# Kernel tuning notes

Measured on AMD Instinct MI355X. Metric: run time of the kernel, lower is better.

The kernel has to match this reference:

```python
import jax, jax.numpy as jnp
import numpy as np

N = 50000   # nodes
E = 800000  # edges (avg degree 16)
D = 2048    # resnet50 feature dim
C = 256     # layer_size
NEG_SLOPE = 0.2


def setup_inputs() -> dict:
    key = jax.random.key(0)
    ks = jax.random.split(key, 16)
    s = 0.02
    inp = {
        'x': jax.random.normal(ks[0], (N, D), jnp.float32),
        'edge_index': jax.random.randint(ks[1], (2, E), 0, N, dtype=jnp.int32),
        # GATConv layer 1 (in=D, out=C, heads=1)
        'W1': jax.random.normal(ks[2], (D, C), jnp.float32) * s,
        'a_src1': jax.random.normal(ks[3], (C,), jnp.float32) * s,
        'a_dst1': jax.random.normal(ks[4], (C,), jnp.float32) * s,
        'b1': jnp.zeros((C,), jnp.float32),
        # GATConv layer 2 (in=C, out=C)
        'W2': jax.random.normal(ks[5], (C, C), jnp.float32) * s,
        'a_src2': jax.random.normal(ks[6], (C,), jnp.float32) * s,
        'a_dst2': jax.random.normal(ks[7], (C,), jnp.float32) * s,
        'b2': jnp.zeros((C,), jnp.float32),
        # EdgePredictor: lin1 (2C -> C), lin2 (C -> 1)
        'Wp1': jax.random.normal(ks[8], (2 * C, C), jnp.float32) * s,
        'bp1': jnp.zeros((C,), jnp.float32),
        'wp2': jax.random.normal(ks[9], (C,), jnp.float32) * s,
        'bp2': jnp.zeros((), jnp.float32),
    }
    return inp


def gat_layer(x, src, dst, W, a_src, a_dst, b, n_nodes):
    # PyG GATConv, heads=1, concat=True: message flows src -> dst,
    # softmax over incoming edges of each dst node.
    h = x @ W                                   # [N, C]
    e = jax.nn.leaky_relu((h @ a_src)[src] + (h @ a_dst)[dst], NEG_SLOPE)  # [E]
    emax = jax.ops.segment_max(e, dst, num_segments=n_nodes)
    ex = jnp.exp(e - emax[dst])
    denom = jax.ops.segment_sum(ex, dst, num_segments=n_nodes)
    alpha = ex / (denom[dst] + 1e-16)           # [E]
    out = jax.ops.segment_sum(h[src] * alpha[:, None], dst, num_segments=n_nodes)
    return out + b


def reference(x, edge_index, W1, a_src1, a_dst1, b1, W2, a_src2, a_dst2, b2,
              Wp1, bp1, wp2, bp2):
    src, dst = edge_index[0], edge_index[1]
    # GATConv default add_self_loops=True
    loops = jnp.arange(N, dtype=src.dtype)
    src_sl = jnp.concatenate([src, loops])
    dst_sl = jnp.concatenate([dst, loops])

    h = gat_layer(x, src_sl, dst_sl, W1, a_src1, a_dst1, b1, N)
    h = gat_layer(h, src_sl, dst_sl, W2, a_src2, a_dst2, b2, N)

    # edge predictor on the ORIGINAL edge_index (no self loops)
    xe = jnp.concatenate([h[src], h[dst]], axis=-1)       # [E, 2C]
    z = jax.nn.relu(xe @ Wp1 + bp1)                        # [E, C]  (dropout: eval mode)
    return z @ wp2 + bp2                                   # [E]
```

## Files before the change

### kernel.cpp

```cpp
#include <hip/hip_runtime.h>
#include <hip/hip_bf16.h>
#include <stdint.h>

#define NNODES 50000
#define NEDGES 800000
#define DIN    2048
#define CDIM   256
#define ELOOP  (NEDGES + NNODES)

using bf16x8 = __attribute__((ext_vector_type(8))) short;
using f32x4  = __attribute__((ext_vector_type(4))) float;
using gvoid  = __attribute__((address_space(1))) const void;
using lvoid  = __attribute__((address_space(3))) void;

__device__ __forceinline__ float bf2f(uint16_t u) {
    union { uint32_t i; float f; } v; v.i = (uint32_t)u << 16; return v.f;
}
__device__ __forceinline__ uint16_t f2bf(float f) {
    union { float f; uint32_t i; } v; v.f = f;
    uint32_t i = v.i;
    return (uint16_t)((i + 0x7FFFu + ((i >> 16) & 1u)) >> 16);
}

#define BM 128
#define BN 128
#define BK 32

#define WAITVM(N) asm volatile("s_waitcnt vmcnt(" #N ")" ::: "memory")

#define ROWDOT_EPILOGUE()                                                     \
    if (s_src) {                                                              \
        float av[4], dv[4];                                                   \
        for (int nt2 = 0; nt2 < 4; ++nt2) {                                   \
            int gn = bn + wn + nt2 * 16 + lm;                                 \
            av[nt2] = asrc[gn];                                               \
            dv[nt2] = adst[gn];                                               \
        }                                                                     \
        for (int mt = 0; mt < 4; ++mt)                                        \
            for (int r = 0; r < 4; ++r) {                                     \
                float ps = 0.f, pd = 0.f;                                     \
                for (int nt2 = 0; nt2 < 4; ++nt2) {                           \
                    float v = acc[mt][nt2][r];                                \
                    ps += v * av[nt2];                                        \
                    pd += v * dv[nt2];                                        \
                }                                                             \
                for (int d = 1; d < 16; d <<= 1) {                            \
                    ps += __shfl_xor(ps, d);                                  \
                    pd += __shfl_xor(pd, d);                                  \
                }                                                             \
                if (lm == 0) {                                                \
                    int gm = bm + wm + mt * 16 + lq * 4 + r;                  \
                    if (gm < M) {                                             \
                        atomicAdd(&s_src[gm], ps);                            \
                        atomicAdd(&s_dst[gm], pd);                            \
                    }                                                         \
                }                                                             \
            }                                                                 \
    }

__global__ __launch_bounds__(256)
void gemm_bt(const uint16_t* __restrict__ A, const uint16_t* __restrict__ Bt,
             uint16_t* __restrict__ C, const float* __restrict__ bias,
             const float* __restrict__ asrc, const float* __restrict__ adst,
             float* __restrict__ s_src, float* __restrict__ s_dst,
             int M, int N, int K)
{
    __shared__ __align__(16) uint16_t lA[3][BM * BK];
    __shared__ __align__(16) uint16_t lB[3][BN * BK];
    const int tid  = threadIdx.x;
    const int wave = tid >> 6;
    const int lane = tid & 63;
    const int lm = lane & 15, lq = lane >> 4;
    const int bm = blockIdx.x * BM;
    const int bn = blockIdx.y * BN;
    const int wm = (wave >> 1) * 64;
    const int wn = (wave & 1) * 64;

    f32x4 acc[4][4];
    for (int i = 0; i < 4; ++i)
        for (int j = 0; j < 4; ++j)
            acc[i][j] = (f32x4)0.0f;

    auto stage = [&](int buf, int k0) {
        for (int j = 0; j < 2; ++j) {
            int c = j * 256 + wave * 64 + lane;
            int row = c >> 2, cc = c & 3;
            int gr = bm + row; if (gr >= M) gr = M - 1;
            const uint16_t* gp = A + (size_t)gr * K + k0 + cc * 8;
            __builtin_amdgcn_global_load_lds((gvoid*)gp,
                (lvoid*)(lA[buf] + (size_t)(j * 256 + wave * 64) * 8), 16, 0, 0);
        }
        for (int j = 0; j < 2; ++j) {
            int c = j * 256 + wave * 64 + lane;
            int row = c >> 2, cc = c & 3;
            const uint16_t* gp = Bt + (size_t)(bn + row) * K + k0 + cc * 8;
            __builtin_amdgcn_global_load_lds((gvoid*)gp,
                (lvoid*)(lB[buf] + (size_t)(j * 256 + wave * 64) * 8), 16, 0, 0);
        }
    };

    const int ntiles = K / BK;
    stage(0, 0);
    stage(1, BK);
    WAITVM(4);
    __builtin_amdgcn_s_barrier();

    for (int t = 0; t < ntiles; ++t) {
        const int cur = t % 3;
        if (t + 2 < ntiles) stage((t + 2) % 3, (t + 2) * BK);

        bf16x8 af[4], bfr[4];
        for (int mt = 0; mt < 4; ++mt)
            af[mt] = *(const bf16x8*)(lA[cur] + (wm + mt * 16 + lm) * BK + lq * 8);
        for (int nt2 = 0; nt2 < 4; ++nt2)
            bfr[nt2] = *(const bf16x8*)(lB[cur] + (wn + nt2 * 16 + lm) * BK + lq * 8);

        for (int mt = 0; mt < 4; ++mt)
            for (int nt2 = 0; nt2 < 4; ++nt2)
                acc[mt][nt2] = __builtin_amdgcn_mfma_f32_16x16x32_bf16(
                    af[mt], bfr[nt2], acc[mt][nt2], 0, 0, 0);

        if (t + 1 < ntiles) {
            if (t + 2 < ntiles) WAITVM(4);
            else                WAITVM(0);
            __builtin_amdgcn_s_barrier();
        }
    }

    for (int mt = 0; mt < 4; ++mt) {
        for (int nt2 = 0; nt2 < 4; ++nt2) {
            int gn = bn + wn + nt2 * 16 + lm;
            float badd = bias ? bias[gn] : 0.0f;
            for (int r = 0; r < 4; ++r) {
                int gm = bm + wm + mt * 16 + lq * 4 + r;
                if (gm < M)
                    C[(size_t)gm * N + gn] = f2bf(acc[mt][nt2][r] + badd);
            }
        }
    }

    ROWDOT_EPILOGUE();
}

__global__ __launch_bounds__(256)
void gemm_f32_bt(const float* __restrict__ A, const uint16_t* __restrict__ Bt,
                 uint16_t* __restrict__ C,
                 const float* __restrict__ asrc, const float* __restrict__ adst,
                 float* __restrict__ s_src, float* __restrict__ s_dst,
                 int M, int N, int K)
{
    __shared__ __align__(16) float    lA[3][BM * BK];
    __shared__ __align__(16) uint16_t lB[3][BN * BK];
    const int tid  = threadIdx.x;
    const int wave = tid >> 6;
    const int lane = tid & 63;
    const int lm = lane & 15, lq = lane >> 4;
    const int bm = blockIdx.x * BM;
    const int bn = blockIdx.y * BN;
    const int wm = (wave >> 1) * 64;
    const int wn = (wave & 1) * 64;

    f32x4 acc[4][4];
    for (int i = 0; i < 4; ++i)
        for (int j = 0; j < 4; ++j)
            acc[i][j] = (f32x4)0.0f;

    auto stage = [&](int buf, int k0) {
        for (int j = 0; j < 4; ++j) {
            int c = j * 256 + wave * 64 + lane;
            int row = c >> 3;
            int lc  = (c & 7) ^ (row & 7);
            int gr = bm + row; if (gr >= M) gr = M - 1;
            const float* gp = A + (size_t)gr * K + k0 + lc * 4;
            __builtin_amdgcn_global_load_lds((gvoid*)gp,
                (lvoid*)(lA[buf] + (size_t)(j * 256 + wave * 64) * 4), 16, 0, 0);
        }
        for (int j = 0; j < 2; ++j) {
            int c = j * 256 + wave * 64 + lane;
            int row = c >> 2, cc = c & 3;
            const uint16_t* gp = Bt + (size_t)(bn + row) * K + k0 + cc * 8;
            __builtin_amdgcn_global_load_lds((gvoid*)gp,
                (lvoid*)(lB[buf] + (size_t)(j * 256 + wave * 64) * 8), 16, 0, 0);
        }
    };

    const int ntiles = K / BK;
    stage(0, 0);
    stage(1, BK);
    WAITVM(6);
    __builtin_amdgcn_s_barrier();

    for (int t = 0; t < ntiles; ++t) {
        const int cur = t % 3;
        if (t + 2 < ntiles) stage((t + 2) % 3, (t + 2) * BK);

        bf16x8 af[4], bfr[4];
        for (int mt = 0; mt < 4; ++mt) {
            int r = wm + mt * 16 + lm;
            int s0 = (lq * 2)     ^ (r & 7);
            int s1 = (lq * 2 + 1) ^ (r & 7);
            f32x4 a0 = *(const f32x4*)(lA[cur] + r * BK + s0 * 4);
            f32x4 a1 = *(const f32x4*)(lA[cur] + r * BK + s1 * 4);
            union { uint32_t u[4]; bf16x8 v; } t2;
            float x0 = a0[0], x1 = a0[1], x2 = a0[2], x3 = a0[3];
            float y0 = a1[0], y1 = a1[1], y2 = a1[2], y3 = a1[3];
            asm("v_cvt_pk_bf16_f32 %0, %1, %2" : "=v"(t2.u[0]) : "v"(x0), "v"(x1));
            asm("v_cvt_pk_bf16_f32 %0, %1, %2" : "=v"(t2.u[1]) : "v"(x2), "v"(x3));
            asm("v_cvt_pk_bf16_f32 %0, %1, %2" : "=v"(t2.u[2]) : "v"(y0), "v"(y1));
            asm("v_cvt_pk_bf16_f32 %0, %1, %2" : "=v"(t2.u[3]) : "v"(y2), "v"(y3));
            af[mt] = t2.v;
        }
        for (int nt2 = 0; nt2 < 4; ++nt2)
            bfr[nt2] = *(const bf16x8*)(lB[cur] + (wn + nt2 * 16 + lm) * BK + lq * 8);

        for (int mt = 0; mt < 4; ++mt)
            for (int nt2 = 0; nt2 < 4; ++nt2)
                acc[mt][nt2] = __builtin_amdgcn_mfma_f32_16x16x32_bf16(
                    af[mt], bfr[nt2], acc[mt][nt2], 0, 0, 0);

        if (t + 1 < ntiles) {
            if (t + 2 < ntiles) WAITVM(6);
            else                WAITVM(0);
            __builtin_amdgcn_s_barrier();
        }
    }

    for (int mt = 0; mt < 4; ++mt) {
        for (int nt2 = 0; nt2 < 4; ++nt2) {
            int gn = bn + wn + nt2 * 16 + lm;
            for (int r = 0; r < 4; ++r) {
                int gm = bm + wm + mt * 16 + lq * 4 + r;
                if (gm < M)
                    C[(size_t)gm * N + gn] = f2bf(acc[mt][nt2][r]);
            }
        }
    }

    ROWDOT_EPILOGUE();
}

__global__ __launch_bounds__(256)
void transpose_cvt_kernel(const float* __restrict__ W,
                          uint16_t* __restrict__ Wt, int K, int N)
{
    __shared__ float tile[32][33];
    const int k0 = blockIdx.x * 32, n0 = blockIdx.y * 32;
    const int tx = threadIdx.x & 31, ty = threadIdx.x >> 5;
    for (int r = 0; r < 32; r += 8)
        tile[ty + r][tx] = W[(size_t)(k0 + ty + r) * N + n0 + tx];
    __syncthreads();
    for (int r = 0; r < 32; r += 8)
        Wt[(size_t)(n0 + ty + r) * K + k0 + tx] = f2bf(tile[tx][ty + r]);
}

__global__ void bias512_kernel(const float* __restrict__ bp1,
                               float* __restrict__ bias512)
{
    int i = blockIdx.x * 256 + threadIdx.x;
    if (i < 512) bias512[i] = (i < 256) ? bp1[i] : 0.0f;
}

__global__ void count_kernel(const int* __restrict__ ei, int* __restrict__ rs)
{
    int i = blockIdx.x * 256 + threadIdx.x;
    if (i >= ELOOP) return;
    int dst = (i < NEDGES) ? ei[NEDGES + i] : (i - NEDGES);
    atomicAdd(&rs[dst + 1], 1);
}

__global__ __launch_bounds__(1024)
void scan_part_kernel(int* __restrict__ rs, int* __restrict__ bsum)
{
    __shared__ int wsum[16];
    const int b = blockIdx.x, tid = threadIdx.x, lane = tid & 63, w = tid >> 6;
    int i = b * 1024 + tid;
    int v = (i <= NNODES) ? rs[i] : 0;
    int s = v;
    for (int d = 1; d < 64; d <<= 1) {
        int t = __shfl_up(s, d);
        if (lane >= d) s += t;
    }
    if (lane == 63) wsum[w] = s;
    __syncthreads();
    if (tid < 16) {
        int x = wsum[tid];
        for (int d = 1; d < 16; d <<= 1) {
            int t = __shfl_up(x, d);
            if (tid >= d) x += t;
        }
        wsum[tid] = x;
    }
    __syncthreads();
    int incl = s + (w > 0 ? wsum[w - 1] : 0);
    if (i <= NNODES) rs[i] = incl;
    if (tid == 1023) bsum[b] = incl;
}

__global__ void scan_bsum_kernel(int* __restrict__ bsum, int nb)
{
    int tid = threadIdx.x;
    int v = (tid < nb) ? bsum[tid] : 0;
    for (int d = 1; d < 64; d <<= 1) {
        int t = __shfl_up(v, d);
        if (tid >= d) v += t;
    }
    if (tid < nb) bsum[tid] = v;
}

__global__ __launch_bounds__(1024)
void scan_add_kernel(const int* __restrict__ bsum, int* __restrict__ rs,
                     int* __restrict__ cursor)
{
    int b = blockIdx.x;
    int i = b * 1024 + threadIdx.x;
    int add = b ? bsum[b - 1] : 0;
    if (i <= NNODES) {
        int r = rs[i] + add;
        rs[i] = r;
        if (i < NNODES) cursor[i] = r;
    }
}

__global__ void fill_kernel(const int* __restrict__ ei, int* __restrict__ cursor,
                            int* __restrict__ csr_src)
{
    int i = blockIdx.x * 256 + threadIdx.x;
    if (i >= ELOOP) return;
    int src, dst;
    if (i < NEDGES) { src = ei[i]; dst = ei[NEDGES + i]; }
    else            { src = dst = i - NEDGES; }
    int pos = atomicAdd(&cursor[dst], 1);
    csr_src[pos] = src;
}

__global__ __launch_bounds__(256)
void attn_kernel(const int* __restrict__ row_start, const int* __restrict__ csr_src,
                 const float* __restrict__ s_src, const float* __restrict__ s_dst,
                 const uint16_t* __restrict__ g, const float* __restrict__ bvec,
                 uint16_t* __restrict__ hout)
{
    int n = blockIdx.x * 4 + (threadIdx.x >> 6);
    int lane = threadIdx.x & 63;
    int h = lane >> 5, hl = lane & 31;
    int beg = row_start[n], end = row_start[n + 1];
    float sdn = s_dst[n];

    float m = -1e30f;
    for (int i = beg + lane; i < end; i += 64) {
        float e = s_src[csr_src[i]] + sdn;
        e = (e > 0.f) ? e : 0.2f * e;
        m = fmaxf(m, e);
    }
    for (int d = 32; d; d >>= 1) m = fmaxf(m, __shfl_xor(m, d));

    float sum = 0.f;
    for (int i = beg + lane; i < end; i += 64) {
        float e = s_src[csr_src[i]] + sdn;
        e = (e > 0.f) ? e : 0.2f * e;
        sum += __expf(e - m);
    }
    for (int d = 32; d; d >>= 1) sum += __shfl_xor(sum, d);
    float inv = 1.f / (sum + 1e-16f);

    float a0 = 0.f, a1 = 0.f, a2 = 0.f, a3 = 0.f;
    float a4 = 0.f, a5 = 0.f, a6 = 0.f, a7 = 0.f;
    for (int i = beg + h; i < end; i += 2) {
        int src = csr_src[i];
        float e = s_src[src] + sdn;
        e = (e > 0.f) ? e : 0.2f * e;
        float alpha = __expf(e - m) * inv;
        uint4 rv = *(const uint4*)(g + (size_t)src * CDIM + hl * 8);
        a0 += alpha * bf2f((uint16_t)(rv.x & 0xffffu));
        a1 += alpha * bf2f((uint16_t)(rv.x >> 16));
        a2 += alpha * bf2f((uint16_t)(rv.y & 0xffffu));
        a3 += alpha * bf2f((uint16_t)(rv.y >> 16));
        a4 += alpha * bf2f((uint16_t)(rv.z & 0xffffu));
        a5 += alpha * bf2f((uint16_t)(rv.z >> 16));
        a6 += alpha * bf2f((uint16_t)(rv.w & 0xffffu));
        a7 += alpha * bf2f((uint16_t)(rv.w >> 16));
    }
    a0 += __shfl_xor(a0, 32); a1 += __shfl_xor(a1, 32);
    a2 += __shfl_xor(a2, 32); a3 += __shfl_xor(a3, 32);
    a4 += __shfl_xor(a4, 32); a5 += __shfl_xor(a5, 32);
    a6 += __shfl_xor(a6, 32); a7 += __shfl_xor(a7, 32);

    if (h == 0) {
        const float4 b0 = *(const float4*)(bvec + hl * 8);
        const float4 b1 = *(const float4*)(bvec + hl * 8 + 4);
        uint4 o;
        o.x = (uint32_t)f2bf(a0 + b0.x) | ((uint32_t)f2bf(a1 + b0.y) << 16);
        o.y = (uint32_t)f2bf(a2 + b0.z) | ((uint32_t)f2bf(a3 + b0.w) << 16);
        o.z = (uint32_t)f2bf(a4 + b1.x) | ((uint32_t)f2bf(a5 + b1.y) << 16);
        o.w = (uint32_t)f2bf(a6 + b1.z) | ((uint32_t)f2bf(a7 + b1.w) << 16);
        *(uint4*)(hout + (size_t)n * CDIM + hl * 8) = o;
    }
}

__global__ __launch_bounds__(256)
void edgepred_kernel(const int* __restrict__ ei,
                     const uint16_t* __restrict__ UV,
                     const float* __restrict__ wp2, const float* __restrict__ bp2,
                     float* __restrict__ out)
{
    const int tid = threadIdx.x;
    const int grp = tid >> 4, l = tid & 15;
    const int e = blockIdx.x * 16 + grp;
    int src = ei[e];
    int dst = ei[NEDGES + e];
    const uint16_t* Up = UV + (size_t)src * 512 + l * 16;
    const uint16_t* Vp = UV + (size_t)dst * 512 + 256 + l * 16;
    const uint4 u0 = *(const uint4*)(Up);
    const uint4 u1 = *(const uint4*)(Up + 8);
    const uint4 v0 = *(const uint4*)(Vp);
    const uint4 v1 = *(const uint4*)(Vp + 8);
    const float4 w0 = *(const float4*)(wp2 + l * 16);
    const float4 w1 = *(const float4*)(wp2 + l * 16 + 4);
    const float4 w2 = *(const float4*)(wp2 + l * 16 + 8);
    const float4 w3 = *(const float4*)(wp2 + l * 16 + 12);
    float acc = 0.f;
    auto proc = [&](uint32_t uu, uint32_t vv, float wa, float wb) {
        float z0 = fmaxf(bf2f((uint16_t)(uu & 0xffffu)) + bf2f((uint16_t)(vv & 0xffffu)), 0.f);
        float z1 = fmaxf(bf2f((uint16_t)(uu >> 16)) + bf2f((uint16_t)(vv >> 16)), 0.f);
        acc += z0 * wa + z1 * wb;
    };
    proc(u0.x, v0.x, w0.x, w0.y); proc(u0.y, v0.y, w0.z, w0.w);
    proc(u0.z, v0.z, w1.x, w1.y); proc(u0.w, v0.w, w1.z, w1.w);
    proc(u1.x, v1.x, w2.x, w2.y); proc(u1.y, v1.y, w2.z, w2.w);
    proc(u1.z, v1.z, w3.x, w3.y); proc(u1.w, v1.w, w3.z, w3.w);
    for (int d = 1; d < 16; d <<= 1) acc += __shfl_xor(acc, d);
    if (l == 0) out[e] = acc + *bp2;
}

extern "C" void kernel_launch(void* const* d_in, const int* in_sizes, int n_in,
                              void* d_out, int out_size, void* d_ws, size_t ws_size,
                              hipStream_t stream)
{
    const float* x   = (const float*)d_in[0];
    const int*   ei  = (const int*)d_in[1];
    const float* W1  = (const float*)d_in[2];
    const float* as1 = (const float*)d_in[3];
    const float* ad1 = (const float*)d_in[4];
    const float* b1  = (const float*)d_in[5];
    const float* W2  = (const float*)d_in[6];
    const float* as2 = (const float*)d_in[7];
    const float* ad2 = (const float*)d_in[8];
    const float* b2  = (const float*)d_in[9];
    const float* Wp1 = (const float*)d_in[10];
    const float* bp1 = (const float*)d_in[11];
    const float* wp2 = (const float*)d_in[12];
    const float* bp2 = (const float*)d_in[13];
    float* out = (float*)d_out;

    char* ws = (char*)d_ws;
    size_t off = 0;
    auto alloc = [&](size_t bytes) -> void* {
        void* p = ws + off;
        off += (bytes + 255) & ~(size_t)255;
        return p;
    };
    uint16_t* W1t   = (uint16_t*)alloc((size_t)DIN * CDIM * 2);
    uint16_t* W2t   = (uint16_t*)alloc((size_t)CDIM * CDIM * 2);
    uint16_t* WpABt = (uint16_t*)alloc((size_t)2 * CDIM * CDIM * 2);
    int* row_start = (int*)alloc((NNODES + 1) * sizeof(int));
    int* cursor    = (int*)alloc(NNODES * sizeof(int));
    int* csr_src   = (int*)alloc((size_t)ELOOP * sizeof(int));
    int* bsum      = (int*)alloc(64 * sizeof(int));
    float* sbuf    = (float*)alloc((size_t)2 * NNODES * sizeof(float));
    float* s_src   = sbuf;
    float* s_dst   = sbuf + NNODES;
    float* bias512 = (float*)alloc(512 * sizeof(float));
    uint16_t* H    = (uint16_t*)alloc((size_t)NNODES * CDIM * 2);
    uint16_t* G    = (uint16_t*)alloc((size_t)NNODES * CDIM * 2);
    uint16_t* Vb   = (uint16_t*)alloc((size_t)NNODES * CDIM * 2);
    (void)Vb;
    uint16_t* UV   = G;

    hipMemsetAsync(row_start, 0, (NNODES + 1) * sizeof(int), stream);
    hipMemsetAsync(sbuf, 0, (size_t)2 * NNODES * sizeof(float), stream);

    transpose_cvt_kernel<<<dim3(DIN / 32, CDIM / 32), 256, 0, stream>>>(W1, W1t, DIN, CDIM);
    transpose_cvt_kernel<<<dim3(CDIM / 32, CDIM / 32), 256, 0, stream>>>(W2, W2t, CDIM, CDIM);
    transpose_cvt_kernel<<<dim3(CDIM / 32, CDIM / 32), 256, 0, stream>>>(Wp1, WpABt, CDIM, CDIM);
    transpose_cvt_kernel<<<dim3(CDIM / 32, CDIM / 32), 256, 0, stream>>>(Wp1 + CDIM * CDIM, WpABt + CDIM * CDIM, CDIM, CDIM);
    bias512_kernel<<<2, 256, 0, stream>>>(bp1, bias512);

    const int NB = (NNODES + 1 + 1023) / 1024;
    count_kernel<<<(ELOOP + 255) / 256, 256, 0, stream>>>(ei, row_start);
    scan_part_kernel<<<NB, 1024, 0, stream>>>(row_start, bsum);
    scan_bsum_kernel<<<1, 64, 0, stream>>>(bsum, NB);
    scan_add_kernel<<<NB, 1024, 0, stream>>>(bsum, row_start, cursor);
    fill_kernel<<<(ELOOP + 255) / 256, 256, 0, stream>>>(ei, cursor, csr_src);

    dim3 gg((NNODES + BM - 1) / BM, CDIM / BN);

    gemm_f32_bt<<<gg, 256, 0, stream>>>(x, W1t, G, as1, ad1, s_src, s_dst,
                                        NNODES, CDIM, DIN);
    attn_kernel<<<NNODES / 4, 256, 0, stream>>>(row_start, csr_src, s_src, s_dst, G, b1, H);

    hipMemsetAsync(sbuf, 0, (size_t)2 * NNODES * sizeof(float), stream);
    gemm_bt<<<gg, 256, 0, stream>>>(H, W2t, G, nullptr, as2, ad2, s_src, s_dst,
                                    NNODES, CDIM, CDIM);
    attn_kernel<<<NNODES / 4, 256, 0, stream>>>(row_start, csr_src, s_src, s_dst, G, b2, H);

    dim3 gg2((NNODES + BM - 1) / BM, 512 / BN);
    gemm_bt<<<gg2, 256, 0, stream>>>(H, WpABt, UV, bias512, nullptr, nullptr,
                                     nullptr, nullptr, NNODES, 512, CDIM);

    edgepred_kernel<<<NEDGES / 16, 256, 0, stream>>>(ei, UV, wp2, bp2, out);
}
```

Before: 1.109 ms.

## Traverse edge predictor by destination CSR and widen attention aggregation lanes

The edge predictor now walks the destination-sorted CSR, one wavefront per node. It loads the destination's V half once and reuses it across all incoming edges, writing results through a stored original edge id; self-loops are marked with -1 and skipped. Output writes become scattered and a second per-edge index array must be written and read. Separately, the attention aggregation splits each wavefront into four groups of 16 lanes, each loading 32 bytes per neighbour row. This processes more edges at once but doubles the accumulator registers and adds a second shuffle stage.

```diff
diff --git a/kernel.cpp b/kernel.cpp
--- a/kernel.cpp
+++ b/kernel.cpp
@@ -20,6 +20,12 @@
     union { float f; uint32_t i; } v; v.f = f;
     uint32_t i = v.i;
     return (uint16_t)((i + 0x7FFFu + ((i >> 16) & 1u)) >> 16);
+}
+__device__ __forceinline__ void unpack8(uint4 r, float* f) {
+    f[0] = bf2f((uint16_t)(r.x & 0xffffu)); f[1] = bf2f((uint16_t)(r.x >> 16));
+    f[2] = bf2f((uint16_t)(r.y & 0xffffu)); f[3] = bf2f((uint16_t)(r.y >> 16));
+    f[4] = bf2f((uint16_t)(r.z & 0xffffu)); f[5] = bf2f((uint16_t)(r.z >> 16));
+    f[6] = bf2f((uint16_t)(r.w & 0xffffu)); f[7] = bf2f((uint16_t)(r.w >> 16));
 }
 
 #define BM 128
@@ -322,15 +328,16 @@
 }
 
 __global__ void fill_kernel(const int* __restrict__ ei, int* __restrict__ cursor,
-                            int* __restrict__ csr_src)
+                            int* __restrict__ csr_src, int* __restrict__ csr_eid)
 {
     int i = blockIdx.x * 256 + threadIdx.x;
     if (i >= ELOOP) return;
-    int src, dst;
-    if (i < NEDGES) { src = ei[i]; dst = ei[NEDGES + i]; }
-    else            { src = dst = i - NEDGES; }
+    int src, dst, eid;
+    if (i < NEDGES) { src = ei[i]; dst = ei[NEDGES + i]; eid = i; }
+    else            { src = dst = i - NEDGES; eid = -1; }
     int pos = atomicAdd(&cursor[dst], 1);
     csr_src[pos] = src;
+    csr_eid[pos] = eid;
 }
 
 __global__ __launch_bounds__(256)
@@ -341,7 +348,6 @@
 {
     int n = blockIdx.x * 4 + (threadIdx.x >> 6);
     int lane = threadIdx.x & 63;
-    int h = lane >> 5, hl = lane & 31;
     int beg = row_start[n], end = row_start[n + 1];
     float sdn = s_dst[n];
 
@@ -362,73 +368,92 @@
     for (int d = 32; d; d >>= 1) sum += __shfl_xor(sum, d);
     float inv = 1.f / (sum + 1e-16f);
 
-    float a0 = 0.f, a1 = 0.f, a2 = 0.f, a3 = 0.f;
-    float a4 = 0.f, a5 = 0.f, a6 = 0.f, a7 = 0.f;
-    for (int i = beg + h; i < end; i += 2) {
+    const int q = lane >> 4, ql = lane & 15;
+    float a[16];
+    #pragma unroll
+    for (int j = 0; j < 16; ++j) a[j] = 0.f;
+
+    for (int i = beg + q; i < end; i += 4) {
         int src = csr_src[i];
         float e = s_src[src] + sdn;
         e = (e > 0.f) ? e : 0.2f * e;
         float alpha = __expf(e - m) * inv;
-        uint4 rv = *(const uint4*)(g + (size_t)src * CDIM + hl * 8);
-        a0 += alpha * bf2f((uint16_t)(rv.x & 0xffffu));
-        a1 += alpha * bf2f((uint16_t)(rv.x >> 16));
-        a2 += alpha * bf2f((uint16_t)(rv.y & 0xffffu));
-        a3 += alpha * bf2f((uint16_t)(rv.y >> 16));
-        a4 += alpha * bf2f((uint16_t)(rv.z & 0xffffu));
-        a5 += alpha * bf2f((uint16_t)(rv.z >> 16));
-        a6 += alpha * bf2f((uint16_t)(rv.w & 0xffffu));
-        a7 += alpha * bf2f((uint16_t)(rv.w >> 16));
-    }
-    a0 += __shfl_xor(a0, 32); a1 += __shfl_xor(a1, 32);
-    a2 += __shfl_xor(a2, 32); a3 += __shfl_xor(a3, 32);
-    a4 += __shfl_xor(a4, 32); a5 += __shfl_xor(a5, 32);
-    a6 += __shfl_xor(a6, 32); a7 += __shfl_xor(a7, 32);
-
-    if (h == 0) {
-        const float4 b0 = *(const float4*)(bvec + hl * 8);
-        const float4 b1 = *(const float4*)(bvec + hl * 8 + 4);
-        uint4 o;
-        o.x = (uint32_t)f2bf(a0 + b0.x) | ((uint32_t)f2bf(a1 + b0.y) << 16);
-        o.y = (uint32_t)f2bf(a2 + b0.z) | ((uint32_t)f2bf(a3 + b0.w) << 16);
-        o.z = (uint32_t)f2bf(a4 + b1.x) | ((uint32_t)f2bf(a5 + b1.y) << 16);
-        o.w = (uint32_t)f2bf(a6 + b1.z) | ((uint32_t)f2bf(a7 + b1.w) << 16);
-        *(uint4*)(hout + (size_t)n * CDIM + hl * 8) = o;
+        const uint16_t* gp = g + (size_t)src * CDIM + ql * 16;
+        uint4 r0 = *(const uint4*)gp;
+        uint4 r1 = *(const uint4*)(gp + 8);
+        float f0[8], f1[8];
+        unpack8(r0, f0); unpack8(r1, f1);
+        #pragma unroll
+        for (int j = 0; j < 8; ++j) {
+            a[j]     += alpha * f0[j];
+            a[8 + j] += alpha * f1[j];
+        }
+    }
+    #pragma unroll
+    for (int j = 0; j < 16; ++j) {
+        a[j] += __shfl_xor(a[j], 16);
+        a[j] += __shfl_xor(a[j], 32);
+    }
+
+    if (q == 0) {
+        const float4 b0 = *(const float4*)(bvec + ql * 16);
+        const float4 b1 = *(const float4*)(bvec + ql * 16 + 4);
+        const float4 b2 = *(const float4*)(bvec + ql * 16 + 8);
+        const float4 b3 = *(const float4*)(bvec + ql * 16 + 12);
+        uint4 o0, o1;
+        o0.x = (uint32_t)f2bf(a[0]  + b0.x) | ((uint32_t)f2bf(a[1]  + b0.y) << 16);
+        o0.y = (uint32_t)f2bf(a[2]  + b0.z) | ((uint32_t)f2bf(a[3]  + b0.w) << 16);
+        o0.z = (uint32_t)f2bf(a[4]  + b1.x) | ((uint32_t)f2bf(a[5]  + b1.y) << 16);
+        o0.w = (uint32_t)f2bf(a[6]  + b1.z) | ((uint32_t)f2bf(a[7]  + b1.w) << 16);
+        o1.x = (uint32_t)f2bf(a[8]  + b2.x) | ((uint32_t)f2bf(a[9]  + b2.y) << 16);
+        o1.y = (uint32_t)f2bf(a[10] + b2.z) | ((uint32_t)f2bf(a[11] + b2.w) << 16);
+        o1.z = (uint32_t)f2bf(a[12] + b3.x) | ((uint32_t)f2bf(a[13] + b3.y) << 16);
+        o1.w = (uint32_t)f2bf(a[14] + b3.z) | ((uint32_t)f2bf(a[15] + b3.w) << 16);
+        uint16_t* op = hout + (size_t)n * CDIM + ql * 16;
+        *(uint4*)op = o0;
+        *(uint4*)(op + 8) = o1;
     }
 }
 
 __global__ __launch_bounds__(256)
-void edgepred_kernel(const int* __restrict__ ei,
+void edgepred_kernel(const int* __restrict__ row_start,
+                     const int* __restrict__ csr_src,
+                     const int* __restrict__ csr_eid,
                      const uint16_t* __restrict__ UV,
                      const float* __restrict__ wp2, const float* __restrict__ bp2,
                      float* __restrict__ out)
 {
-    const int tid = threadIdx.x;
-    const int grp = tid >> 4, l = tid & 15;
-    const int e = blockIdx.x * 16 + grp;
-    int src = ei[e];
-    int dst = ei[NEDGES + e];
-    const uint16_t* Up = UV + (size_t)src * 512 + l * 16;
-    const uint16_t* Vp = UV + (size_t)dst * 512 + 256 + l * 16;
-    const uint4 u0 = *(const uint4*)(Up);
-    const uint4 u1 = *(const uint4*)(Up + 8);
-    const uint4 v0 = *(const uint4*)(Vp);
-    const uint4 v1 = *(const uint4*)(Vp + 8);
-    const float4 w0 = *(const float4*)(wp2 + l * 16);
-    const float4 w1 = *(const float4*)(wp2 + l * 16 + 4);
-    const float4 w2 = *(const float4*)(wp2 + l * 16 + 8);
-    const float4 w3 = *(const float4*)(wp2 + l * 16 + 12);
-    float acc = 0.f;
-    auto proc = [&](uint32_t uu, uint32_t vv, float wa, float wb) {
-        float z0 = fmaxf(bf2f((uint16_t)(uu & 0xffffu)) + bf2f((uint16_t)(vv & 0xffffu)), 0.f);
-        float z1 = fmaxf(bf2f((uint16_t)(uu >> 16)) + bf2f((uint16_t)(vv >> 16)), 0.f);
-        acc += z0 * wa + z1 * wb;
-    };
-    proc(u0.x, v0.x, w0.x, w0.y); proc(u0.y, v0.y, w0.z, w0.w);
-    proc(u0.z, v0.z, w1.x, w1.y); proc(u0.w, v0.w, w1.z, w1.w);
-    proc(u1.x, v1.x, w2.x, w2.y); proc(u1.y, v1.y, w2.z, w2.w);
-    proc(u1.z, v1.z, w3.x, w3.y); proc(u1.w, v1.w, w3.z, w3.w);
-    for (int d = 1; d < 16; d <<= 1) acc += __shfl_xor(acc, d);
-    if (l == 0) out[e] = acc + *bp2;
+    int n = blockIdx.x * 4 + (threadIdx.x >> 6);
+    int lane = threadIdx.x & 63;
+    int h = lane >> 5, hl = lane & 31;
+    int beg = row_start[n], end = row_start[n + 1];
+
+    uint4 vv = *(const uint4*)(UV + (size_t)n * 512 + 256 + hl * 8);
+    float v[8];
+    unpack8(vv, v);
+    const float4 wa = *(const float4*)(wp2 + hl * 8);
+    const float4 wb = *(const float4*)(wp2 + hl * 8 + 4);
+    const float bp = *bp2;
+
+    for (int i = beg + h; i < end; i += 2) {
+        int eid = csr_eid[i];
+        if (eid < 0) continue;
+        int src = csr_src[i];
+        uint4 uu = *(const uint4*)(UV + (size_t)src * 512 + hl * 8);
+        float u[8];
+        unpack8(uu, u);
+        float acc;
+        {
+            float z0 = fmaxf(u[0] + v[0], 0.f), z1 = fmaxf(u[1] + v[1], 0.f);
+            float z2 = fmaxf(u[2] + v[2], 0.f), z3 = fmaxf(u[3] + v[3], 0.f);
+            float z4 = fmaxf(u[4] + v[4], 0.f), z5 = fmaxf(u[5] + v[5], 0.f);
+            float z6 = fmaxf(u[6] + v[6], 0.f), z7 = fmaxf(u[7] + v[7], 0.f);
+            acc = z0 * wa.x + z1 * wa.y + z2 * wa.z + z3 * wa.w
+                + z4 * wb.x + z5 * wb.y + z6 * wb.z + z7 * wb.w;
+        }
+        for (int d = 1; d < 32; d <<= 1) acc += __shfl_xor(acc, d);
+        if (hl == 0) out[eid] = acc + bp;
+    }
 }
 
 extern "C" void kernel_launch(void* const* d_in, const int* in_sizes, int n_in,
@@ -464,6 +489,7 @@
     int* row_start = (int*)alloc((NNODES + 1) * sizeof(int));
     int* cursor    = (int*)alloc(NNODES * sizeof(int));
     int* csr_src   = (int*)alloc((size_t)ELOOP * sizeof(int));
+    int* csr_eid   = (int*)alloc((size_t)ELOOP * sizeof(int));
     int* bsum      = (int*)alloc(64 * sizeof(int));
     float* sbuf    = (float*)alloc((size_t)2 * NNODES * sizeof(float));
     float* s_src   = sbuf;
@@ -489,7 +515,7 @@
     scan_part_kernel<<<NB, 1024, 0, stream>>>(row_start, bsum);
     scan_bsum_kernel<<<1, 64, 0, stream>>>(bsum, NB);
     scan_add_kernel<<<NB, 1024, 0, stream>>>(bsum, row_start, cursor);
-    fill_kernel<<<(ELOOP + 255) / 256, 256, 0, stream>>>(ei, cursor, csr_src);
+    fill_kernel<<<(ELOOP + 255) / 256, 256, 0, stream>>>(ei, cursor, csr_src, csr_eid);
 
     dim3 gg((NNODES + BM - 1) / BM, CDIM / BN);
 
@@ -506,5 +532,6 @@
     gemm_bt<<<gg2, 256, 0, stream>>>(H, WpABt, UV, bias512, nullptr, nullptr,
                                      nullptr, nullptr, NNODES, 512, CDIM);
 
-    edgepred_kernel<<<NEDGES / 16, 256, 0, stream>>>(ei, UV, wp2, bp2, out);
-}
+    edgepred_kernel<<<NNODES / 4, 256, 0, stream>>>(row_start, csr_src, csr_eid,
+                                                    UV, wp2, bp2, out);
+}
```

Result: faster. 1.086 ms (-2.1%).
